# Optimization experiments

Measured on AMD Instinct MI355X. Metric: run time of the kernel, lower is better.

The kernel has to match this reference:

```python
import jax, jax.numpy as jnp
import numpy as np

B, S, HID = 1, 2048, 2880
H, HKV, D = 64, 8, 64
WINDOW = 128
SCALE = D ** -0.5
NEG = -1e30


def _rope(x, cos, sin):
    # x: [B, S, h, D]; cos/sin: [S, D//2]; interleaved complex rotation
    x1 = x[..., 0::2]
    x2 = x[..., 1::2]
    c = cos[None, :, None, :]
    s = sin[None, :, None, :]
    o1 = x1 * c - x2 * s
    o2 = x1 * s + x2 * c
    out = jnp.stack([o1, o2], axis=-1)  # [B,S,h,D/2,2]
    return out.reshape(x.shape)


def setup_inputs() -> dict:
    key = jax.random.key(0)
    ks = jax.random.split(key, 12)
    x = jax.random.normal(ks[0], (B, S, HID), dtype=jnp.float32)
    # rotary tables (head_dim/2 frequencies)
    inv_freq = 1.0 / (10000.0 ** (np.arange(0, D, 2, dtype=np.float32) / D))
    t = np.arange(S, dtype=np.float32)
    ang = np.outer(t, inv_freq)  # [S, D/2]
    cos = jnp.asarray(np.cos(ang))
    sin = jnp.asarray(np.sin(ang))
    std = 0.02
    Wq = jax.random.normal(ks[1], (HID, H * D), dtype=jnp.float32) * std
    bq = jnp.zeros((H * D,), dtype=jnp.float32)
    Wk = jax.random.normal(ks[2], (HID, HKV * D), dtype=jnp.float32) * std
    bk = jnp.zeros((HKV * D,), dtype=jnp.float32)
    Wv = jax.random.normal(ks[3], (HID, HKV * D), dtype=jnp.float32) * std
    bv = jnp.zeros((HKV * D,), dtype=jnp.float32)
    Wo = jax.random.normal(ks[4], (H * D, HID), dtype=jnp.float32) * std
    bo = jnp.zeros((HID,), dtype=jnp.float32)
    sinks = jax.random.normal(ks[5], (H,), dtype=jnp.float32) * std
    return {"x": x, "cos": cos, "sin": sin, "Wq": Wq, "bq": bq,
            "Wk": Wk, "bk": bk, "Wv": Wv, "bv": bv, "Wo": Wo, "bo": bo,
            "sinks": sinks}


def reference(x, cos, sin, Wq, bq, Wk, bk, Wv, bv, Wo, bo, sinks):
    b, s, _ = x.shape
    q = (x @ Wq + bq).reshape(b, s, H, D)
    k = (x @ Wk + bk).reshape(b, s, HKV, D)
    v = (x @ Wv + bv).reshape(b, s, HKV, D)
    q = _rope(q, cos, sin)
    k = _rope(k, cos, sin)
    # GQA: expand kv heads to H
    rep = H // HKV
    k = jnp.repeat(k, rep, axis=2)  # [B,S,H,D]
    v = jnp.repeat(v, rep, axis=2)
    scores = jnp.einsum("bqhd,bkhd->bhqk", q, k) * SCALE  # [B,H,S,S]
    i = jnp.arange(s)[:, None]
    j = jnp.arange(s)[None, :]
    mask = (j <= i) & (i - j < WINDOW)  # causal sliding window
    z = jnp.where(mask[None, None], scores, NEG)
    sink = sinks[None, :, None]  # [1,H,1] extra logit per head
    m = jnp.maximum(jnp.max(z, axis=-1), sink)  # [B,H,S]
    p = jnp.exp(z - m[..., None])
    denom = jnp.sum(p, axis=-1) + jnp.exp(sink - m)  # [B,H,S]
    out = jnp.einsum("bhqk,bkhd->bhqd", p, v) / denom[..., None]
    out = out.transpose(0, 2, 1, 3).reshape(b, s, H * D)
    return out @ Wo + bo
```

## Files before the change

### kernel.cpp

```cpp
#include <hip/hip_runtime.h>
#include <stdint.h>

#define S_LEN   2048
#define HID_DIM 2880
#define NHEAD   64
#define NKVH    8
#define DHEAD   64
#define NQ      4096
#define NKVD    512
#define NQKV    5120
#define WOPAD   2944
#define ATT_SCALE 0.125f
#define NEGINF  (-1e30f)

typedef __attribute__((ext_vector_type(8))) short bf16x8;
typedef __attribute__((ext_vector_type(4))) float f32x4;

typedef __attribute__((address_space(3))) uint32_t lds_u32;
typedef const __attribute__((address_space(1))) uint32_t glb_u32;

__device__ __forceinline__ void gl_lds16(const short* g, short* l) {
  __builtin_amdgcn_global_load_lds((glb_u32*)(uintptr_t)g,
                                   (lds_u32*)(uint32_t)(uintptr_t)l, 16, 0, 0);
}

__device__ __forceinline__ short f2bf(float f) {
  union { float f; uint32_t u; } c; c.f = f;
  uint32_t u = c.u;
  return (short)((u + 0x7FFFu + ((u >> 16) & 1u)) >> 16);
}

__global__ void k_cvt_x(const float* __restrict__ src, short* __restrict__ dst, int n4) {
  int i = blockIdx.x * 256 + threadIdx.x;
  if (i >= n4) return;
  float4 v = ((const float4*)src)[i];
  short4 o;
  o.x = f2bf(v.x); o.y = f2bf(v.y); o.z = f2bf(v.z); o.w = f2bf(v.w);
  ((short4*)dst)[i] = o;
}

__global__ void k_transpose_cvt(const float* __restrict__ src, short* __restrict__ dst,
                                int K, int N) {
  __shared__ float tile[32][33];
  int k0 = blockIdx.x * 32, n0 = blockIdx.y * 32;
  int tx = threadIdx.x, ty = threadIdx.y;
#pragma unroll
  for (int j = 0; j < 4; ++j) {
    int n = n0 + tx, k = k0 + ty + j * 8;
    tile[ty + j * 8][tx] = (n < N) ? src[(size_t)k * N + n] : 0.f;
  }
  __syncthreads();
#pragma unroll
  for (int j = 0; j < 4; ++j) {
    int n = n0 + ty + j * 8;
    dst[(size_t)n * K + k0 + tx] = f2bf(tile[tx][ty + j * 8]);
  }
}

template <int EPI>
__global__ __launch_bounds__(512) void k_gemm(
    const short* __restrict__ A, const short* __restrict__ B, int K,
    const float* __restrict__ biasq, const float* __restrict__ biask,
    const float* __restrict__ biasv,
    const float* __restrict__ cosT, const float* __restrict__ sinT,
    short* __restrict__ qout, short* __restrict__ kout, short* __restrict__ vout,
    const float* __restrict__ bo, float* __restrict__ out) {
  const int tid = threadIdx.x;
  const int lane = tid & 63, wid = tid >> 6;
  const int wm = wid >> 2, wn = wid & 3;
  const int l15 = lane & 15, lhi = lane >> 4;
  const int row0 = blockIdx.y * 128, col0 = blockIdx.x * 128;

  __shared__ short As[128 * 64];
  __shared__ short Bs[128 * 64];

  f32x4 acc[4][2];
#pragma unroll
  for (int i = 0; i < 4; ++i)
#pragma unroll
    for (int j = 0; j < 2; ++j) acc[i][j] = (f32x4){0.f, 0.f, 0.f, 0.f};

  const short* aSrc[2];
  const short* bSrc[2];
  int dOff[2];
#pragma unroll
  for (int i = 0; i < 2; ++i) {
    int p = i * 512 + tid;
    int m = p >> 3, slot = p & 7;
    int ss = slot ^ (m & 7);
    aSrc[i] = A + (size_t)(row0 + m) * K + ss * 8;
    bSrc[i] = B + (size_t)(col0 + m) * K + ss * 8;
    dOff[i] = p * 8;
  }

  const int nkt = K >> 6;
  for (int kt = 0; kt < nkt; ++kt) {
    __syncthreads();
#pragma unroll
    for (int i = 0; i < 2; ++i) gl_lds16(aSrc[i] + kt * 64, &As[dOff[i]]);
#pragma unroll
    for (int i = 0; i < 2; ++i) gl_lds16(bSrc[i] + kt * 64, &Bs[dOff[i]]);
    __syncthreads();
#pragma unroll
    for (int kk = 0; kk < 2; ++kk) {
      bf16x8 af[4], bf[2];
#pragma unroll
      for (int mi = 0; mi < 4; ++mi) {
        int r = wm * 64 + mi * 16 + l15;
        int sl = (kk * 4 + lhi) ^ (r & 7);
        af[mi] = *(const bf16x8*)((char*)As + r * 128 + sl * 16);
      }
#pragma unroll
      for (int ni = 0; ni < 2; ++ni) {
        int r = wn * 32 + ni * 16 + l15;
        int sl = (kk * 4 + lhi) ^ (r & 7);
        bf[ni] = *(const bf16x8*)((char*)Bs + r * 128 + sl * 16);
      }
#pragma unroll
      for (int mi = 0; mi < 4; ++mi)
#pragma unroll
        for (int ni = 0; ni < 2; ++ni)
          acc[mi][ni] = __builtin_amdgcn_mfma_f32_16x16x32_bf16(af[mi], bf[ni], acc[mi][ni], 0, 0, 0);
    }
  }

  if (EPI == 0) {
#pragma unroll
    for (int mi = 0; mi < 4; ++mi) {
#pragma unroll
      for (int r = 0; r < 4; ++r) {
        int mg = row0 + wm * 64 + mi * 16 + lhi * 4 + r;
#pragma unroll
        for (int ni = 0; ni < 2; ++ni) {
          int ng = col0 + wn * 32 + ni * 16 + l15;
          float v = acc[mi][ni][r];
          v += (ng < NQ) ? biasq[ng] : (ng < NQ + NKVD ? biask[ng - NQ] : biasv[ng - NQ - NKVD]);
          if (ng < NQ + NKVD) {
            float partner = __shfl_xor(v, 1);
            int d = ng & 63, p = d >> 1;
            float c = cosT[mg * 32 + p], s = sinT[mg * 32 + p];
            v = (d & 1) ? (partner * s + v * c) : (v * c - partner * s);
          }
          short b16 = f2bf(v);
          if (ng < NQ)              qout[(size_t)mg * NQ + ng] = b16;
          else if (ng < NQ + NKVD)  kout[(size_t)mg * NKVD + (ng - NQ)] = b16;
          else                      vout[(size_t)mg * NKVD + (ng - NQ - NKVD)] = b16;
        }
      }
    }
  } else {
#pragma unroll
    for (int mi = 0; mi < 4; ++mi) {
#pragma unroll
      for (int r = 0; r < 4; ++r) {
        int mg = row0 + wm * 64 + mi * 16 + lhi * 4 + r;
#pragma unroll
        for (int ni = 0; ni < 2; ++ni) {
          int ng = col0 + wn * 32 + ni * 16 + l15;
          if (ng < HID_DIM) out[(size_t)mg * HID_DIM + ng] = acc[mi][ni][r] + bo[ng];
        }
      }
    }
  }
}

__global__ __launch_bounds__(256) void k_attn(
    const short* __restrict__ qb, const short* __restrict__ kb,
    const short* __restrict__ vb, const float* __restrict__ sinks,
    short* __restrict__ attnb) {
  const int h = blockIdx.x & 63;
  const int q0 = (blockIdx.x >> 6) * 64;
  const int tid = threadIdx.x;
  const int lane = tid & 63, wq = tid >> 6;
  const int l15 = lane & 15, lhi = lane >> 4;
  const int hkv = h >> 3;
  const int kstart = q0 - 128;

  __shared__ short Vt[64 * 256];
  __shared__ short Plds[4][16 * 168];

  {
    int d = tid >> 2;
    int k16 = (tid & 3) * 16;
#pragma unroll
    for (int j = 0; j < 16; j += 4)
      *(short4*)&Vt[d * 256 + 192 + k16 + j] = (short4){0, 0, 0, 0};
  }

  {
    int krow = tid >> 2;
    int dbase = (tid & 3) * 16;
#pragma unroll
    for (int rep = 0; rep < 3; ++rep) {
      int key = rep * 64 + krow;
      int gk = kstart + key;
      int gkc = gk < 0 ? 0 : gk;
      const short* src = vb + (size_t)gkc * NKVD + hkv * 64 + dbase;
      uint4 v0 = *(const uint4*)(src);
      uint4 v1 = *(const uint4*)(src + 8);
      uint32_t w[8] = {v0.x, v0.y, v0.z, v0.w, v1.x, v1.y, v1.z, v1.w};
#pragma unroll
      for (int i = 0; i < 8; ++i) {
        int d0 = dbase + 2 * i, d1 = dbase + 2 * i + 1;
        Vt[d0 * 256 + (key ^ ((d0 & 7) << 3))] = (short)(w[i] & 0xffffu);
        Vt[d1 * 256 + (key ^ ((d1 & 7) << 3))] = (short)(w[i] >> 16);
      }
    }
  }

  int qrow = q0 + wq * 16 + l15;
  bf16x8 aq[2];
#pragma unroll
  for (int kk = 0; kk < 2; ++kk)
    aq[kk] = *(const bf16x8*)(qb + (size_t)qrow * NQ + h * 64 + kk * 32 + lhi * 8);

  f32x4 sacc[9];
#pragma unroll
  for (int ni = 0; ni < 9; ++ni) {
    int key = kstart + (wq + ni) * 16 + l15;
    int keyc = key < 0 ? 0 : key;
    const short* kp = kb + (size_t)keyc * NKVD + hkv * 64;
    bf16x8 b0 = *(const bf16x8*)(kp + lhi * 8);
    bf16x8 b1 = *(const bf16x8*)(kp + 32 + lhi * 8);
    f32x4 z = (f32x4){0.f, 0.f, 0.f, 0.f};
    z = __builtin_amdgcn_mfma_f32_16x16x32_bf16(aq[0], b0, z, 0, 0, 0);
    z = __builtin_amdgcn_mfma_f32_16x16x32_bf16(aq[1], b1, z, 0, 0, 0);
    sacc[ni] = z;
  }

  float snk = sinks[h];
  float mx[4] = {NEGINF, NEGINF, NEGINF, NEGINF};
#pragma unroll
  for (int ni = 0; ni < 9; ++ni) {
    int j = kstart + (wq + ni) * 16 + l15;
#pragma unroll
    for (int r = 0; r < 4; ++r) {
      int iq = q0 + wq * 16 + lhi * 4 + r;
      float sv = sacc[ni][r] * ATT_SCALE;
      bool valid = (j >= 0) && (j <= iq) && (iq - j < 128);
      sv = valid ? sv : NEGINF;
      sacc[ni][r] = sv;
      mx[r] = fmaxf(mx[r], sv);
    }
  }
#pragma unroll
  for (int r = 0; r < 4; ++r) {
    float m = mx[r];
    m = fmaxf(m, __shfl_xor(m, 1));
    m = fmaxf(m, __shfl_xor(m, 2));
    m = fmaxf(m, __shfl_xor(m, 4));
    m = fmaxf(m, __shfl_xor(m, 8));
    mx[r] = fmaxf(m, snk);
  }
  float sm[4] = {0.f, 0.f, 0.f, 0.f};
#pragma unroll
  for (int ni = 0; ni < 9; ++ni)
#pragma unroll
    for (int r = 0; r < 4; ++r) {
      float p = __expf(sacc[ni][r] - mx[r]);
      sacc[ni][r] = p;
      sm[r] += p;
    }
  float inv[4];
#pragma unroll
  for (int r = 0; r < 4; ++r) {
    float s = sm[r];
    s += __shfl_xor(s, 1);
    s += __shfl_xor(s, 2);
    s += __shfl_xor(s, 4);
    s += __shfl_xor(s, 8);
    s += __expf(snk - mx[r]);
    inv[r] = 1.0f / s;
  }

  short* pw = &Plds[wq][0];
#pragma unroll
  for (int ni = 0; ni < 9; ++ni)
#pragma unroll
    for (int r = 0; r < 4; ++r)
      pw[(lhi * 4 + r) * 168 + ni * 16 + l15] = f2bf(sacc[ni][r]);
#pragma unroll
  for (int r = 0; r < 4; ++r)
    pw[(lhi * 4 + r) * 168 + 144 + l15] = 0;

  __syncthreads();

  f32x4 oacc[4];
#pragma unroll
  for (int nt = 0; nt < 4; ++nt) oacc[nt] = (f32x4){0.f, 0.f, 0.f, 0.f};
  const short* pr = &Plds[wq][0];
#pragma unroll
  for (int ks = 0; ks < 5; ++ks) {
    bf16x8 pf = *(const bf16x8*)(pr + l15 * 168 + ks * 32 + lhi * 8);
#pragma unroll
    for (int nt = 0; nt < 4; ++nt) {
      int d = nt * 16 + l15;
      int keyidx = wq * 16 + ks * 32 + lhi * 8;
      bf16x8 vf = *(const bf16x8*)(&Vt[d * 256 + (keyidx ^ ((d & 7) << 3))]);
      oacc[nt] = __builtin_amdgcn_mfma_f32_16x16x32_bf16(pf, vf, oacc[nt], 0, 0, 0);
    }
  }

#pragma unroll
  for (int nt = 0; nt < 4; ++nt)
#pragma unroll
    for (int r = 0; r < 4; ++r) {
      int iq = q0 + wq * 16 + lhi * 4 + r;
      int d = nt * 16 + l15;
      attnb[(size_t)iq * NQ + h * 64 + d] = f2bf(oacc[nt][r] * inv[r]);
    }
}

extern "C" void kernel_launch(void* const* d_in, const int* in_sizes, int n_in,
                              void* d_out, int out_size, void* d_ws, size_t ws_size,
                              hipStream_t stream) {
  const float* x     = (const float*)d_in[0];
  const float* cosT  = (const float*)d_in[1];
  const float* sinT  = (const float*)d_in[2];
  const float* Wq    = (const float*)d_in[3];
  const float* bq    = (const float*)d_in[4];
  const float* Wk    = (const float*)d_in[5];
  const float* bk    = (const float*)d_in[6];
  const float* Wv    = (const float*)d_in[7];
  const float* bv    = (const float*)d_in[8];
  const float* Wo    = (const float*)d_in[9];
  const float* bo    = (const float*)d_in[10];
  const float* sinks = (const float*)d_in[11];
  float* out = (float*)d_out;

  short* xb    = (short*)d_ws;
  short* wqkvb = xb + (size_t)S_LEN * HID_DIM;
  short* wob   = wqkvb + (size_t)NQKV * HID_DIM;
  short* qbuf  = wob + (size_t)WOPAD * NQ;
  short* kbuf  = qbuf + (size_t)S_LEN * NQ;
  short* vbuf  = kbuf + (size_t)S_LEN * NKVD;
  short* attnb = vbuf + (size_t)S_LEN * NKVD;

  dim3 tb(32, 8);
  k_cvt_x<<<(S_LEN * HID_DIM / 4 + 255) / 256, 256, 0, stream>>>(x, xb, S_LEN * HID_DIM / 4);
  k_transpose_cvt<<<dim3(HID_DIM / 32, NQ / 32), tb, 0, stream>>>(Wq, wqkvb, HID_DIM, NQ);
  k_transpose_cvt<<<dim3(HID_DIM / 32, NKVD / 32), tb, 0, stream>>>(Wk, wqkvb + (size_t)NQ * HID_DIM, HID_DIM, NKVD);
  k_transpose_cvt<<<dim3(HID_DIM / 32, NKVD / 32), tb, 0, stream>>>(Wv, wqkvb + (size_t)(NQ + NKVD) * HID_DIM, HID_DIM, NKVD);
  k_transpose_cvt<<<dim3(NQ / 32, WOPAD / 32), tb, 0, stream>>>(Wo, wob, NQ, HID_DIM);

  k_gemm<0><<<dim3(NQKV / 128, S_LEN / 128), 512, 0, stream>>>(
      xb, wqkvb, HID_DIM, bq, bk, bv, cosT, sinT, qbuf, kbuf, vbuf, nullptr, nullptr);

  k_attn<<<(S_LEN / 64) * NHEAD, 256, 0, stream>>>(qbuf, kbuf, vbuf, sinks, attnb);

  k_gemm<1><<<dim3(WOPAD / 128, S_LEN / 128), 512, 0, stream>>>(
      attnb, wob, NQ, nullptr, nullptr, nullptr, nullptr, nullptr,
      nullptr, nullptr, nullptr, bo, out);
}
```

Baseline: 230.7 us.

## Fuse prep kernels, shrink GEMM tiles to 64x128, add XCD-aware block swizzle

Merges the x conversion and the four weight transpose-convert launches into one k_prep kernel, which cuts launch overhead. Shrinks the GEMM workgroup tile from 128x128 with 8 waves to 64x128 with 4 waves, doubling the number of blocks so the many CUs are better filled. Adds a block-index swizzle that groups consecutive tiles onto the same XCD for L2 reuse. Smaller tiles lower per-block operand reuse, and the hardcoded block counts in k_prep tie it to the fixed shapes.

```diff
diff --git a/kernel.cpp b/kernel.cpp
--- a/kernel.cpp
+++ b/kernel.cpp
@@ -30,20 +30,37 @@
   return (short)((u + 0x7FFFu + ((u >> 16) & 1u)) >> 16);
 }
 
-__global__ void k_cvt_x(const float* __restrict__ src, short* __restrict__ dst, int n4) {
-  int i = blockIdx.x * 256 + threadIdx.x;
-  if (i >= n4) return;
-  float4 v = ((const float4*)src)[i];
-  short4 o;
-  o.x = f2bf(v.x); o.y = f2bf(v.y); o.z = f2bf(v.z); o.w = f2bf(v.w);
-  ((short4*)dst)[i] = o;
-}
-
-__global__ void k_transpose_cvt(const float* __restrict__ src, short* __restrict__ dst,
-                                int K, int N) {
+__global__ __launch_bounds__(256) void k_prep(
+    const float* __restrict__ x, short* __restrict__ xb,
+    const float* __restrict__ Wq, const float* __restrict__ Wk,
+    const float* __restrict__ Wv, const float* __restrict__ Wo,
+    short* __restrict__ wqkvb, short* __restrict__ wob) {
+  int b = blockIdx.x;
+  if (b < 5760) {
+    int i = b * 256 + threadIdx.x;
+    float4 v = ((const float4*)x)[i];
+    short4 o;
+    o.x = f2bf(v.x); o.y = f2bf(v.y); o.z = f2bf(v.z); o.w = f2bf(v.w);
+    ((short4*)xb)[i] = o;
+    return;
+  }
+  b -= 5760;
+  const float* src; short* dst; int K, N, tk;
+  if (b < 11520) {
+    src = Wq; dst = wqkvb; K = 2880; N = 4096; tk = 90;
+  } else if (b < 11520 + 1440) {
+    b -= 11520;
+    src = Wk; dst = wqkvb + (size_t)NQ * HID_DIM; K = 2880; N = 512; tk = 90;
+  } else if (b < 11520 + 2880) {
+    b -= 11520 + 1440;
+    src = Wv; dst = wqkvb + (size_t)(NQ + NKVD) * HID_DIM; K = 2880; N = 512; tk = 90;
+  } else {
+    b -= 11520 + 2880;
+    src = Wo; dst = wob; K = 4096; N = 2880; tk = 128;
+  }
+  int k0 = (b % tk) * 32, n0 = (b / tk) * 32;
   __shared__ float tile[32][33];
-  int k0 = blockIdx.x * 32, n0 = blockIdx.y * 32;
-  int tx = threadIdx.x, ty = threadIdx.y;
+  int tx = threadIdx.x & 31, ty = threadIdx.x >> 5;
 #pragma unroll
   for (int j = 0; j < 4; ++j) {
     int n = n0 + tx, k = k0 + ty + j * 8;
@@ -58,7 +75,7 @@
 }
 
 template <int EPI>
-__global__ __launch_bounds__(512) void k_gemm(
+__global__ __launch_bounds__(256) void k_gemm(
     const short* __restrict__ A, const short* __restrict__ B, int K,
     const float* __restrict__ biasq, const float* __restrict__ biask,
     const float* __restrict__ biasv,
@@ -66,12 +83,18 @@
     short* __restrict__ qout, short* __restrict__ kout, short* __restrict__ vout,
     const float* __restrict__ bo, float* __restrict__ out) {
   const int tid = threadIdx.x;
-  const int lane = tid & 63, wid = tid >> 6;
-  const int wm = wid >> 2, wn = wid & 3;
+  const int lane = tid & 63, wn = tid >> 6;
   const int l15 = lane & 15, lhi = lane >> 4;
-  const int row0 = blockIdx.y * 128, col0 = blockIdx.x * 128;
-
-  __shared__ short As[128 * 64];
+
+  const int nbx = gridDim.x;
+  const int nwg = nbx * gridDim.y;
+  const int bid = blockIdx.y * nbx + blockIdx.x;
+  const int qc = nwg >> 3, rc = nwg & 7;
+  const int xcd = bid & 7, idx = bid >> 3;
+  const int swz = (xcd < rc ? xcd * (qc + 1) : rc * (qc + 1) + (xcd - rc) * qc) + idx;
+  const int row0 = (swz / nbx) * 64, col0 = (swz % nbx) * 128;
+
+  __shared__ short As[64 * 64];
   __shared__ short Bs[128 * 64];
 
   f32x4 acc[4][2];
@@ -80,33 +103,39 @@
 #pragma unroll
     for (int j = 0; j < 2; ++j) acc[i][j] = (f32x4){0.f, 0.f, 0.f, 0.f};
 
-  const short* aSrc[2];
-  const short* bSrc[2];
-  int dOff[2];
+  const short* aSrc[2]; int aOff[2];
+  const short* bSrc[4]; int bOff[4];
 #pragma unroll
   for (int i = 0; i < 2; ++i) {
-    int p = i * 512 + tid;
+    int p = i * 256 + tid;
     int m = p >> 3, slot = p & 7;
     int ss = slot ^ (m & 7);
     aSrc[i] = A + (size_t)(row0 + m) * K + ss * 8;
+    aOff[i] = p * 8;
+  }
+#pragma unroll
+  for (int i = 0; i < 4; ++i) {
+    int p = i * 256 + tid;
+    int m = p >> 3, slot = p & 7;
+    int ss = slot ^ (m & 7);
     bSrc[i] = B + (size_t)(col0 + m) * K + ss * 8;
-    dOff[i] = p * 8;
+    bOff[i] = p * 8;
   }
 
   const int nkt = K >> 6;
   for (int kt = 0; kt < nkt; ++kt) {
     __syncthreads();
 #pragma unroll
-    for (int i = 0; i < 2; ++i) gl_lds16(aSrc[i] + kt * 64, &As[dOff[i]]);
-#pragma unroll
-    for (int i = 0; i < 2; ++i) gl_lds16(bSrc[i] + kt * 64, &Bs[dOff[i]]);
+    for (int i = 0; i < 2; ++i) gl_lds16(aSrc[i] + kt * 64, &As[aOff[i]]);
+#pragma unroll
+    for (int i = 0; i < 4; ++i) gl_lds16(bSrc[i] + kt * 64, &Bs[bOff[i]]);
     __syncthreads();
 #pragma unroll
     for (int kk = 0; kk < 2; ++kk) {
       bf16x8 af[4], bf[2];
 #pragma unroll
       for (int mi = 0; mi < 4; ++mi) {
-        int r = wm * 64 + mi * 16 + l15;
+        int r = mi * 16 + l15;
         int sl = (kk * 4 + lhi) ^ (r & 7);
         af[mi] = *(const bf16x8*)((char*)As + r * 128 + sl * 16);
       }
@@ -129,7 +158,7 @@
     for (int mi = 0; mi < 4; ++mi) {
 #pragma unroll
       for (int r = 0; r < 4; ++r) {
-        int mg = row0 + wm * 64 + mi * 16 + lhi * 4 + r;
+        int mg = row0 + mi * 16 + lhi * 4 + r;
 #pragma unroll
         for (int ni = 0; ni < 2; ++ni) {
           int ng = col0 + wn * 32 + ni * 16 + l15;
@@ -153,7 +182,7 @@
     for (int mi = 0; mi < 4; ++mi) {
 #pragma unroll
       for (int r = 0; r < 4; ++r) {
-        int mg = row0 + wm * 64 + mi * 16 + lhi * 4 + r;
+        int mg = row0 + mi * 16 + lhi * 4 + r;
 #pragma unroll
         for (int ni = 0; ni < 2; ++ni) {
           int ng = col0 + wn * 32 + ni * 16 + l15;
@@ -336,19 +365,14 @@
   short* vbuf  = kbuf + (size_t)S_LEN * NKVD;
   short* attnb = vbuf + (size_t)S_LEN * NKVD;
 
-  dim3 tb(32, 8);
-  k_cvt_x<<<(S_LEN * HID_DIM / 4 + 255) / 256, 256, 0, stream>>>(x, xb, S_LEN * HID_DIM / 4);
-  k_transpose_cvt<<<dim3(HID_DIM / 32, NQ / 32), tb, 0, stream>>>(Wq, wqkvb, HID_DIM, NQ);
-  k_transpose_cvt<<<dim3(HID_DIM / 32, NKVD / 32), tb, 0, stream>>>(Wk, wqkvb + (size_t)NQ * HID_DIM, HID_DIM, NKVD);
-  k_transpose_cvt<<<dim3(HID_DIM / 32, NKVD / 32), tb, 0, stream>>>(Wv, wqkvb + (size_t)(NQ + NKVD) * HID_DIM, HID_DIM, NKVD);
-  k_transpose_cvt<<<dim3(NQ / 32, WOPAD / 32), tb, 0, stream>>>(Wo, wob, NQ, HID_DIM);
-
-  k_gemm<0><<<dim3(NQKV / 128, S_LEN / 128), 512, 0, stream>>>(
+  k_prep<<<31936, 256, 0, stream>>>(x, xb, Wq, Wk, Wv, Wo, wqkvb, wob);
+
+  k_gemm<0><<<dim3(NQKV / 128, S_LEN / 64), 256, 0, stream>>>(
       xb, wqkvb, HID_DIM, bq, bk, bv, cosT, sinT, qbuf, kbuf, vbuf, nullptr, nullptr);
 
   k_attn<<<(S_LEN / 64) * NHEAD, 256, 0, stream>>>(qbuf, kbuf, vbuf, sinks, attnb);
 
-  k_gemm<1><<<dim3(WOPAD / 128, S_LEN / 128), 512, 0, stream>>>(
+  k_gemm<1><<<dim3(WOPAD / 128, S_LEN / 64), 256, 0, stream>>>(
       attnb, wob, NQ, nullptr, nullptr, nullptr, nullptr, nullptr,
       nullptr, nullptr, nullptr, bo, out);
 }
```

Result: slower. 247.9 us (+7.4%).
